# Performance work log

Measured on AMD Instinct MI355X. Metric: run time of the kernel, lower is better.

## Reference

```python
import jax, jax.numpy as jnp
import numpy as np
import math

K = 7
SIGMA1, SIGMA2 = 2.5, 1.0


def _gaussian_kernel(size, sigma1, sigma2, theta):
    ax = np.linspace(-(size // 2), size // 2, size, dtype=np.float32)
    xx, yy = np.meshgrid(ax, ax, indexing='ij')
    x_rot = xx * math.cos(theta) + yy * math.sin(theta)
    y_rot = -xx * math.sin(theta) + yy * math.cos(theta)
    k = np.exp(-(x_rot ** 2 / (2 * sigma1 ** 2) + y_rot ** 2 / (2 * sigma2 ** 2)))
    return (k / k.sum()).astype(np.float32)


def _base_kernels():
    angles = [0.0, math.pi / 4, math.pi / 2, 3 * math.pi / 4]
    return np.stack([_gaussian_kernel(K, SIGMA1, SIGMA2, t) for t in angles], axis=0)  # (4,K,K)


def setup_inputs() -> dict:
    key = jax.random.key(0)
    ks = jax.random.split(key, 6)
    B, C, H, W = 8, 128, 128, 128
    x = jax.random.normal(ks[0], (B, C, H, W), dtype=jnp.float32)
    angle_map = jax.random.uniform(ks[1], (B, H, W), dtype=jnp.float32) * jnp.float32(math.pi)
    # weight_net: Linear(2,8) -> ReLU -> Linear(8,4) -> Softmax
    w1 = jax.random.normal(ks[2], (8, 2), dtype=jnp.float32) * 0.5
    b1 = jax.random.normal(ks[3], (8,), dtype=jnp.float32) * 0.1
    w2 = jax.random.normal(ks[4], (4, 8), dtype=jnp.float32) * 0.3
    b2 = jax.random.normal(ks[5], (4,), dtype=jnp.float32) * 0.1
    base_kernels = jnp.asarray(_base_kernels())  # (4,K,K), deterministic buffer
    return {"x": x, "angle_map": angle_map, "w1": w1, "b1": b1,
            "w2": w2, "b2": b2, "base_kernels": base_kernels}


def reference(x, angle_map, w1, b1, w2, b2, base_kernels):
    # x: (B,C,H,W); angle_map: (B,H,W); base_kernels: (4,K,K)
    B, C, H, W = x.shape
    k = base_kernels.shape[-1]
    pad = k // 2
    # Per-pixel mixing weights over the 4 directional base kernels.
    feat = jnp.stack([jnp.sin(2.0 * angle_map), jnp.cos(2.0 * angle_map)], axis=-1)  # (B,H,W,2)
    h = jax.nn.relu(jnp.einsum('bhwi,oi->bhwo', feat, w1) + b1)
    weights = jax.nn.softmax(jnp.einsum('bhwi,oi->bhwo', h, w2) + b2, axis=-1)  # (B,H,W,4)
    # The original forms combined[b,h,w,kh,kw] = sum_d weights[...d] * base[d] and applies it
    # via unfold+einsum. Correlation is linear in the kernel, so equivalently:
    # out = sum_d weights[...,d] * depthwise_corr(x_reflectpad, base[d])  -- same math, no unfold.
    xp = jnp.pad(x, ((0, 0), (0, 0), (pad, pad), (pad, pad)), mode='reflect')
    xr = xp.reshape(B * C, 1, H + 2 * pad, W + 2 * pad)
    ker = base_kernels[:, None, :, :]  # (4,1,K,K)
    y = jax.lax.conv_general_dilated(
        xr, ker, window_strides=(1, 1), padding='VALID',
        dimension_numbers=('NCHW', 'OIHW', 'NCHW'))  # (B*C,4,H,W)
    y = y.reshape(B, C, 4, H, W)
    return jnp.einsum('bcdhw,bhwd->bchw', y, weights)
```

## Files before the change

kernel.cpp:

```cpp
#include <hip/hip_runtime.h>
#include <math.h>

#define B_   8
#define C_   128
#define H_   128
#define W_   128
#define TX   32
#define TY   32
#define VPX  4
#define PAD  3
#define HX   (TX + 2*PAD)
#define HY   (TY + 2*PAD)
#define NPOS (HX*HY)
#define NC   4
#define CPB  32
#define NGRP (CPB/NC)
#define NCHUNK (C_/CPB)
#define NSLOT 6
#define REM  (NPOS - 5*256)

struct KTab { float sk[4][25]; };

__device__ __forceinline__ int refl(int i, int n) {
    if (i < 0) i = -i;
    if (i >= n) i = 2*n - 2 - i;
    return i;
}

__global__ __launch_bounds__(256, 2) void ddconv_kernel(
    const float* __restrict__ x,
    const float* __restrict__ angle,
    const float* __restrict__ w1,
    const float* __restrict__ b1,
    const float* __restrict__ w2,
    const float* __restrict__ b2,
    float* __restrict__ out,
    KTab kt)
{
    __shared__ float4 buf[2][NPOS];

    const int tid = threadIdx.x;
    const int tx  = tid & 31;
    const int tr  = tid >> 5;
    const int bx  = blockIdx.x;
    const int TX0 = (bx & 3) * TX;
    const int TY0 = (bx >> 2) * TY;
    const int b   = blockIdx.y;
    const int c0  = blockIdx.z * CPB;
    const int y0  = TY0 + VPX*tr;
    const int wv  = TX0 + tx;
    const size_t HW = (size_t)H_ * W_;

    int off[NSLOT];
#pragma unroll
    for (int s = 0; s < NSLOT; ++s) {
        int p = tid + s*256;
        if (p >= NPOS) p = NPOS - 1;
        int gy = refl(TY0 + p/HX - PAD, H_);
        int gx = refl(TX0 + p%HX - PAD, W_);
        off[s] = gy*W_ + gx;
    }
    const bool hasR = (tid < REM);

    float4 pv[NSLOT];
    {
        const float* xb = x + ((size_t)(b*C_ + c0))*HW;
#pragma unroll
        for (int s = 0; s < NSLOT; ++s) {
            if (s == NSLOT-1 && !hasR) break;
            pv[s].x = xb[0*HW + off[s]]; pv[s].y = xb[1*HW + off[s]];
            pv[s].z = xb[2*HW + off[s]]; pv[s].w = xb[3*HW + off[s]];
        }
    }

    float wt[VPX][4];
#pragma unroll
    for (int p = 0; p < VPX; ++p) {
        float a = angle[((size_t)b*H_ + (y0+p))*W_ + wv];
        float s = __sinf(2.f*a), c = __cosf(2.f*a);
        float hv[8];
#pragma unroll
        for (int j = 0; j < 8; ++j) {
            float v = fmaf(s, w1[2*j], fmaf(c, w1[2*j+1], b1[j]));
            hv[j] = v > 0.f ? v : 0.f;
        }
        float lg[4];
#pragma unroll
        for (int d = 0; d < 4; ++d) {
            float v = b2[d];
#pragma unroll
            for (int j = 0; j < 8; ++j) v = fmaf(hv[j], w2[d*8+j], v);
            lg[d] = v;
        }
        float m  = fmaxf(fmaxf(lg[0], lg[1]), fmaxf(lg[2], lg[3]));
        float e0 = __expf(lg[0]-m), e1 = __expf(lg[1]-m);
        float e2 = __expf(lg[2]-m), e3 = __expf(lg[3]-m);
        float inv = 1.f / (e0+e1+e2+e3);
        wt[p][0] = e0*inv; wt[p][1] = e1*inv; wt[p][2] = e2*inv; wt[p][3] = e3*inv;
    }

    float kb[VPX][25];
#pragma unroll
    for (int u = 0; u < 25; ++u) {
        const float s0 = kt.sk[0][u], s1 = kt.sk[1][u];
        const float s2 = kt.sk[2][u], s3 = kt.sk[3][u];
#pragma unroll
        for (int p = 0; p < VPX; ++p)
            kb[p][u] = wt[p][0]*s0 + wt[p][1]*s1 + wt[p][2]*s2 + wt[p][3]*s3;
    }

#pragma unroll
    for (int s = 0; s < NSLOT; ++s) {
        if (s == NSLOT-1 && !hasR) break;
        buf[0][tid + s*256] = pv[s];
    }

    for (int g = 0; g < NGRP; ++g) {
        __syncthreads();

        const bool doStage = (g + 1 < NGRP);
        if (doStage) {
            const float* xb = x + ((size_t)(b*C_ + c0 + (g+1)*NC))*HW;
#pragma unroll
            for (int s = 0; s < NSLOT; ++s) {
                if (s == NSLOT-1 && !hasR) break;
                pv[s].x = xb[0*HW + off[s]]; pv[s].y = xb[1*HW + off[s]];
                pv[s].z = xb[2*HW + off[s]]; pv[s].w = xb[3*HW + off[s]];
            }
        }

        const float4* tb = buf[g & 1];
        float4 acc[VPX];
#pragma unroll
        for (int p = 0; p < VPX; ++p) acc[p] = (float4){0.f,0.f,0.f,0.f};

#pragma unroll
        for (int r = 0; r < VPX + 6; ++r) {
            float4 win[7];
            const int base = (VPX*tr + r)*HX + tx;
#pragma unroll
            for (int j = 0; j < 7; ++j) win[j] = tb[base + j];
#pragma unroll
            for (int p = 0; p < VPX; ++p) {
                const int i = r - p;
                if (i < 0 || i > 6) continue;
#pragma unroll
                for (int j = 0; j < 7; ++j) {
                    const int t = i*7 + j;
                    const int u = (t <= 24) ? t : 48 - t;
                    const float k = kb[p][u];
                    acc[p].x = fmaf(win[j].x, k, acc[p].x);
                    acc[p].y = fmaf(win[j].y, k, acc[p].y);
                    acc[p].z = fmaf(win[j].z, k, acc[p].z);
                    acc[p].w = fmaf(win[j].w, k, acc[p].w);
                }
            }
        }

        float* ob = out + ((size_t)(b*C_ + c0 + g*NC))*HW + (size_t)y0*W_ + wv;
#pragma unroll
        for (int p = 0; p < VPX; ++p) {
            ob[p*W_ + 0*HW] = acc[p].x;
            ob[p*W_ + 1*HW] = acc[p].y;
            ob[p*W_ + 2*HW] = acc[p].z;
            ob[p*W_ + 3*HW] = acc[p].w;
        }

        if (doStage) {
            float4* nb = buf[(g+1) & 1];
#pragma unroll
            for (int s = 0; s < NSLOT; ++s) {
                if (s == NSLOT-1 && !hasR) break;
                nb[tid + s*256] = pv[s];
            }
        }
    }
}

static KTab make_ktab() {
    KTab t;
    const double sig1 = 2.5, sig2 = 1.0;
    const double angles[4] = {0.0, M_PI/4.0, M_PI/2.0, 3.0*M_PI/4.0};
    for (int d = 0; d < 4; ++d) {
        double th = angles[d], cs = cos(th), sn = sin(th);
        double sum = 0.0, k[7][7];
        for (int i = 0; i < 7; ++i) for (int j = 0; j < 7; ++j) {
            double xx = i - 3, yy = j - 3;
            double xr = xx*cs + yy*sn, yr = -xx*sn + yy*cs;
            k[i][j] = exp(-(xr*xr/(2.0*sig1*sig1) + yr*yr/(2.0*sig2*sig2)));
            sum += k[i][j];
        }
        for (int u = 0; u < 25; ++u)
            t.sk[d][u] = (float)(k[u/7][u%7]/sum);
    }
    return t;
}

extern "C" void kernel_launch(void* const* d_in, const int* in_sizes, int n_in,
                              void* d_out, int out_size, void* d_ws, size_t ws_size,
                              hipStream_t stream) {
    const float* x     = (const float*)d_in[0];
    const float* angle = (const float*)d_in[1];
    const float* w1    = (const float*)d_in[2];
    const float* b1    = (const float*)d_in[3];
    const float* w2    = (const float*)d_in[4];
    const float* b2    = (const float*)d_in[5];
    float* out = (float*)d_out;

    static const KTab kt = make_ktab();

    dim3 grid((W_/TX)*(H_/TY), B_, NCHUNK);
    dim3 block(256);
    ddconv_kernel<<<grid, block, 0, stream>>>(x, angle, w1, b1, w2, b2, out, kt);
}
```

Baseline: 50.20 us.

## Stage input tile in fp16 LDS and compute 2x2 outputs per thread

Converts staged input to packed fp16 in shared memory, which halves LDS footprint and read traffic. Each thread now computes a 2x2 output patch instead of a 4x1 column, and stores results as float2. Channels per block drop from 32 to 16 and occupancy target rises to 3 blocks per SM. This trades input precision (fp16 round-toward-zero) for bandwidth, risks accuracy tolerance, and doubles the halo reload ratio per channel.

```diff
diff --git a/kernel.cpp b/kernel.cpp
--- a/kernel.cpp
+++ b/kernel.cpp
@@ -5,20 +5,19 @@
 #define C_   128
 #define H_   128
 #define W_   128
-#define TX   32
-#define TY   32
-#define VPX  4
+#define TS   32
 #define PAD  3
-#define HX   (TX + 2*PAD)
-#define HY   (TY + 2*PAD)
-#define NPOS (HX*HY)
+#define HS   (TS + 2*PAD)
+#define NPOS (HS*HS)
 #define NC   4
-#define CPB  32
+#define CPB  16
 #define NGRP (CPB/NC)
 #define NCHUNK (C_/CPB)
 #define NSLOT 6
 #define REM  (NPOS - 5*256)
 
+typedef _Float16 h8 __attribute__((ext_vector_type(8)));
+
 struct KTab { float sk[4][25]; };
 
 __device__ __forceinline__ int refl(int i, int n) {
@@ -27,7 +26,13 @@
     return i;
 }
 
-__global__ __launch_bounds__(256, 2) void ddconv_kernel(
+__device__ __forceinline__ uint2 pack4(const float4& v) {
+    unsigned lo = __builtin_bit_cast(unsigned, __builtin_amdgcn_cvt_pkrtz(v.x, v.y));
+    unsigned hi = __builtin_bit_cast(unsigned, __builtin_amdgcn_cvt_pkrtz(v.z, v.w));
+    return make_uint2(lo, hi);
+}
+
+__global__ __launch_bounds__(256, 3) void ddconv_kernel(
     const float* __restrict__ x,
     const float* __restrict__ angle,
     const float* __restrict__ w1,
@@ -37,18 +42,18 @@
     float* __restrict__ out,
     KTab kt)
 {
-    __shared__ float4 buf[2][NPOS];
+    __shared__ __align__(16) uint2 sb[2][NPOS];
 
     const int tid = threadIdx.x;
-    const int tx  = tid & 31;
-    const int tr  = tid >> 5;
+    const int tx2 = tid & 15;
+    const int ty2 = tid >> 4;
     const int bx  = blockIdx.x;
-    const int TX0 = (bx & 3) * TX;
-    const int TY0 = (bx >> 2) * TY;
+    const int TX0 = (bx & 3) * TS;
+    const int TY0 = (bx >> 2) * TS;
     const int b   = blockIdx.y;
     const int c0  = blockIdx.z * CPB;
-    const int y0  = TY0 + VPX*tr;
-    const int wv  = TX0 + tx;
+    const int ox  = TX0 + 2*tx2;
+    const int oy  = TY0 + 2*ty2;
     const size_t HW = (size_t)H_ * W_;
 
     int off[NSLOT];
@@ -56,8 +61,8 @@
     for (int s = 0; s < NSLOT; ++s) {
         int p = tid + s*256;
         if (p >= NPOS) p = NPOS - 1;
-        int gy = refl(TY0 + p/HX - PAD, H_);
-        int gx = refl(TX0 + p%HX - PAD, W_);
+        int gy = refl(TY0 + p/HS - PAD, H_);
+        int gx = refl(TX0 + p%HS - PAD, W_);
         off[s] = gy*W_ + gx;
     }
     const bool hasR = (tid < REM);
@@ -73,46 +78,55 @@
         }
     }
 
-    float wt[VPX][4];
-#pragma unroll
-    for (int p = 0; p < VPX; ++p) {
-        float a = angle[((size_t)b*H_ + (y0+p))*W_ + wv];
-        float s = __sinf(2.f*a), c = __cosf(2.f*a);
-        float hv[8];
-#pragma unroll
-        for (int j = 0; j < 8; ++j) {
-            float v = fmaf(s, w1[2*j], fmaf(c, w1[2*j+1], b1[j]));
-            hv[j] = v > 0.f ? v : 0.f;
-        }
-        float lg[4];
-#pragma unroll
-        for (int d = 0; d < 4; ++d) {
-            float v = b2[d];
-#pragma unroll
-            for (int j = 0; j < 8; ++j) v = fmaf(hv[j], w2[d*8+j], v);
-            lg[d] = v;
-        }
-        float m  = fmaxf(fmaxf(lg[0], lg[1]), fmaxf(lg[2], lg[3]));
-        float e0 = __expf(lg[0]-m), e1 = __expf(lg[1]-m);
-        float e2 = __expf(lg[2]-m), e3 = __expf(lg[3]-m);
-        float inv = 1.f / (e0+e1+e2+e3);
-        wt[p][0] = e0*inv; wt[p][1] = e1*inv; wt[p][2] = e2*inv; wt[p][3] = e3*inv;
-    }
-
-    float kb[VPX][25];
+    float wt[2][2][4];
+#pragma unroll
+    for (int p = 0; p < 2; ++p) {
+        float2 a2 = *reinterpret_cast<const float2*>(
+            &angle[((size_t)b*H_ + (oy+p))*W_ + ox]);
+#pragma unroll
+        for (int h = 0; h < 2; ++h) {
+            float a = (h == 0) ? a2.x : a2.y;
+            float s = __sinf(2.f*a), c = __cosf(2.f*a);
+            float hv[8];
+#pragma unroll
+            for (int j = 0; j < 8; ++j) {
+                float v = fmaf(s, w1[2*j], fmaf(c, w1[2*j+1], b1[j]));
+                hv[j] = v > 0.f ? v : 0.f;
+            }
+            float lg[4];
+#pragma unroll
+            for (int d = 0; d < 4; ++d) {
+                float v = b2[d];
+#pragma unroll
+                for (int j = 0; j < 8; ++j) v = fmaf(hv[j], w2[d*8+j], v);
+                lg[d] = v;
+            }
+            float m  = fmaxf(fmaxf(lg[0], lg[1]), fmaxf(lg[2], lg[3]));
+            float e0 = __expf(lg[0]-m), e1 = __expf(lg[1]-m);
+            float e2 = __expf(lg[2]-m), e3 = __expf(lg[3]-m);
+            float inv = 1.f / (e0+e1+e2+e3);
+            wt[p][h][0] = e0*inv; wt[p][h][1] = e1*inv;
+            wt[p][h][2] = e2*inv; wt[p][h][3] = e3*inv;
+        }
+    }
+
+    float kb[2][2][25];
 #pragma unroll
     for (int u = 0; u < 25; ++u) {
         const float s0 = kt.sk[0][u], s1 = kt.sk[1][u];
         const float s2 = kt.sk[2][u], s3 = kt.sk[3][u];
 #pragma unroll
-        for (int p = 0; p < VPX; ++p)
-            kb[p][u] = wt[p][0]*s0 + wt[p][1]*s1 + wt[p][2]*s2 + wt[p][3]*s3;
+        for (int p = 0; p < 2; ++p)
+#pragma unroll
+            for (int h = 0; h < 2; ++h)
+                kb[p][h][u] = wt[p][h][0]*s0 + wt[p][h][1]*s1
+                            + wt[p][h][2]*s2 + wt[p][h][3]*s3;
     }
 
 #pragma unroll
     for (int s = 0; s < NSLOT; ++s) {
         if (s == NSLOT-1 && !hasR) break;
-        buf[0][tid + s*256] = pv[s];
+        sb[0][tid + s*256] = pack4(pv[s]);
     }
 
     for (int g = 0; g < NGRP; ++g) {
@@ -129,49 +143,60 @@
             }
         }
 
-        const float4* tb = buf[g & 1];
-        float4 acc[VPX];
-#pragma unroll
-        for (int p = 0; p < VPX; ++p) acc[p] = (float4){0.f,0.f,0.f,0.f};
-
-#pragma unroll
-        for (int r = 0; r < VPX + 6; ++r) {
-            float4 win[7];
-            const int base = (VPX*tr + r)*HX + tx;
-#pragma unroll
-            for (int j = 0; j < 7; ++j) win[j] = tb[base + j];
-#pragma unroll
-            for (int p = 0; p < VPX; ++p) {
+        float acc[2][2][4];
+#pragma unroll
+        for (int p = 0; p < 2; ++p)
+#pragma unroll
+            for (int h = 0; h < 2; ++h)
+#pragma unroll
+                for (int ch = 0; ch < 4; ++ch) acc[p][h][ch] = 0.f;
+
+#pragma unroll
+        for (int r = 0; r < 8; ++r) {
+            const h8* wp = reinterpret_cast<const h8*>(
+                &sb[g & 1][(2*ty2 + r)*HS + 2*tx2]);
+            h8 Wc[4];
+#pragma unroll
+            for (int c = 0; c < 4; ++c) Wc[c] = wp[c];
+#pragma unroll
+            for (int p = 0; p < 2; ++p) {
                 const int i = r - p;
                 if (i < 0 || i > 6) continue;
 #pragma unroll
                 for (int j = 0; j < 7; ++j) {
                     const int t = i*7 + j;
                     const int u = (t <= 24) ? t : 48 - t;
-                    const float k = kb[p][u];
-                    acc[p].x = fmaf(win[j].x, k, acc[p].x);
-                    acc[p].y = fmaf(win[j].y, k, acc[p].y);
-                    acc[p].z = fmaf(win[j].z, k, acc[p].z);
-                    acc[p].w = fmaf(win[j].w, k, acc[p].w);
+#pragma unroll
+                    for (int h = 0; h < 2; ++h) {
+                        const int pos = j + h;
+                        const float k = kb[p][h][u];
+#pragma unroll
+                        for (int ch = 0; ch < 4; ++ch) {
+                            float xv = (float)Wc[pos >> 1][(pos & 1)*4 + ch];
+                            acc[p][h][ch] = fmaf(xv, k, acc[p][h][ch]);
+                        }
+                    }
                 }
             }
         }
 
-        float* ob = out + ((size_t)(b*C_ + c0 + g*NC))*HW + (size_t)y0*W_ + wv;
-#pragma unroll
-        for (int p = 0; p < VPX; ++p) {
-            ob[p*W_ + 0*HW] = acc[p].x;
-            ob[p*W_ + 1*HW] = acc[p].y;
-            ob[p*W_ + 2*HW] = acc[p].z;
-            ob[p*W_ + 3*HW] = acc[p].w;
+#pragma unroll
+        for (int ch = 0; ch < 4; ++ch) {
+            float* ob = out + ((size_t)(b*C_ + c0 + g*NC + ch))*HW
+                            + (size_t)oy*W_ + ox;
+#pragma unroll
+            for (int p = 0; p < 2; ++p) {
+                float2 st = {acc[p][0][ch], acc[p][1][ch]};
+                *reinterpret_cast<float2*>(&ob[p*W_]) = st;
+            }
         }
 
         if (doStage) {
-            float4* nb = buf[(g+1) & 1];
+            uint2* nb = sb[(g+1) & 1];
 #pragma unroll
             for (int s = 0; s < NSLOT; ++s) {
                 if (s == NSLOT-1 && !hasR) break;
-                nb[tid + s*256] = pv[s];
+                nb[tid + s*256] = pack4(pv[s]);
             }
         }
     }
@@ -209,7 +234,7 @@
 
     static const KTab kt = make_ktab();
 
-    dim3 grid((W_/TX)*(H_/TY), B_, NCHUNK);
+    dim3 grid((W_/TS)*(H_/TS), B_, NCHUNK);
     dim3 block(256);
     ddconv_kernel<<<grid, block, 0, stream>>>(x, angle, w1, b1, w2, b2, out, kt);
 }
```

Result: slower. 106.2 us (+111.5%).
